# Kernel tuning notes

Hardware: AMD Instinct MI355X
Metric: run time of the kernel (lower is better)

The kernel has to match this reference:

```python
import jax, jax.numpy as jnp
import numpy as np

NHEAD, D_K, D_V, D_MODEL = 16, 64, 64, 1024
B, LQ, LK = 2, 2048, 2048
LN_EPS = 1e-6


def setup_inputs() -> dict:
    key = jax.random.key(0)
    ks = jax.random.split(key, 12)
    s = 0.02
    return {
        "q": jax.random.normal(ks[0], (B, LQ, D_MODEL), jnp.float32),
        "k": jax.random.normal(ks[1], (B, LK, D_MODEL), jnp.float32),
        "v": jax.random.normal(ks[2], (B, LK, D_MODEL), jnp.float32),
        "mask": jax.random.randint(ks[3], (B, LQ, LK), 0, 2, jnp.int32),
        "mean": jax.random.uniform(ks[4], (B, LK), jnp.float32, 0.5, 1.5),
        "std": jax.random.uniform(ks[5], (B, LK), jnp.float32, -0.5, 0.5),
        "w_qs": jax.random.normal(ks[6], (D_MODEL, NHEAD * D_K), jnp.float32) * s,
        "w_ks": jax.random.normal(ks[7], (D_MODEL, NHEAD * D_K), jnp.float32) * s,
        "w_vs": jax.random.normal(ks[8], (D_MODEL, NHEAD * D_V), jnp.float32) * s,
        "w_fc": jax.random.normal(ks[9], (NHEAD * D_V, D_MODEL), jnp.float32) * s,
        "ln_gamma": jnp.ones((D_MODEL,), jnp.float32),
        "ln_beta": jnp.zeros((D_MODEL,), jnp.float32),
    }


def _layer_norm(x, gamma, beta):
    mu = jnp.mean(x, axis=-1, keepdims=True)
    var = jnp.mean(jnp.square(x - mu), axis=-1, keepdims=True)
    return (x - mu) * jax.lax.rsqrt(var + LN_EPS) * gamma + beta


def reference(q, k, v, mask, mean, std, w_qs, w_ks, w_vs, w_fc, ln_gamma, ln_beta):
    residual = q
    # projections -> [B, H, L, d]
    qh = (q @ w_qs).reshape(B, LQ, NHEAD, D_K).transpose(0, 2, 1, 3)
    kh = (k @ w_ks).reshape(B, LK, NHEAD, D_K).transpose(0, 2, 1, 3)
    vh = (v @ w_vs).reshape(B, LK, NHEAD, D_V).transpose(0, 2, 1, 3)
    # scores with affine modification: (QK^T * mean + std) / sqrt(d_k)
    attn = jnp.einsum("bhqd,bhkd->bhqk", qh, kh)
    attn = (attn * mean[:, None, None, :] + std[:, None, None, :]) / jnp.sqrt(jnp.float32(D_K))
    attn = jnp.where(mask[:, None, :, :] == 0, jnp.float32(-1e9), attn)
    attn = jax.nn.softmax(attn, axis=-1)
    out = jnp.einsum("bhqk,bhkd->bhqd", attn, vh)  # [B,H,Lq,Dv]
    out = out.transpose(0, 2, 1, 3).reshape(B, LQ, NHEAD * D_V)
    out = out @ w_fc + residual
    return _layer_norm(out, ln_gamma, ln_beta)
```

## Files before the change

### kernel.cpp

```cpp
#include <hip/hip_runtime.h>
#include <math.h>

#define NHEAD 16
#define DK 64
#define DMODEL 1024
#define BB 2
#define LQ 2048
#define LK 2048
#define MROWS (BB * LQ)

typedef __attribute__((ext_vector_type(8))) short short8v;
typedef __attribute__((ext_vector_type(4))) float f32x4;
typedef __attribute__((ext_vector_type(16))) float f32x16;

__device__ __forceinline__ ushort f2bf(float x) {
  uint u = __builtin_bit_cast(uint, x);
  u += 0x7FFFu + ((u >> 16) & 1u);
  return (ushort)(u >> 16);
}
__device__ __forceinline__ float bf2f(ushort h) {
  return __builtin_bit_cast(float, ((uint)h) << 16);
}

template <int MODE>
__global__ __launch_bounds__(256, 2) void gemm_mfma(
    const float* __restrict__ A, const float* __restrict__ W,
    float* __restrict__ out, const float* __restrict__ res) {
  __shared__ __align__(16) ushort As_hi[128 * 32], As_lo[128 * 32];
  __shared__ __align__(16) ushort Bs_hi[128 * 32], Bs_lo[128 * 32];

  const int t = threadIdx.x;
  const int ln = t & 63, wv = t >> 6;
  const int wm = wv >> 1, wn = wv & 1;
  const int n0 = blockIdx.x * 128, m0 = blockIdx.y * 128;

  const int am = t & 127, akg = t >> 7;
  const int bn = t & 127, bkg = t >> 7;

  const float* Ap = A + (size_t)(m0 + am) * 1024 + akg * 16;
  const float* Wp = W + (size_t)(bkg * 16) * 1024 + n0 + bn;

  float4 apf[4];
  float wpf[16];
#pragma unroll
  for (int q = 0; q < 4; ++q) apf[q] = *(const float4*)&Ap[q * 4];
#pragma unroll
  for (int j = 0; j < 16; ++j) wpf[j] = Wp[(size_t)j * 1024];

  f32x4 acc[4][4];
#pragma unroll
  for (int i = 0; i < 4; ++i)
#pragma unroll
    for (int j = 0; j < 4; ++j)
#pragma unroll
      for (int r = 0; r < 4; ++r) acc[i][j][r] = 0.f;

  for (int k0 = 0; k0 < 1024; k0 += 32) {
    __syncthreads();
    {
      ushort h8[16], l8[16];
#pragma unroll
      for (int q = 0; q < 4; ++q)
#pragma unroll
        for (int c = 0; c < 4; ++c) {
          float x = apf[q][c];
          ushort hb = f2bf(x);
          h8[q * 4 + c] = hb;
          l8[q * 4 + c] = f2bf(x - bf2f(hb));
        }
      const int sw = (am >> 1) & 3;
      short8v va0, va1, vb0, vb1;
#pragma unroll
      for (int i = 0; i < 8; ++i) {
        va0[i] = (short)h8[i]; va1[i] = (short)h8[8 + i];
        vb0[i] = (short)l8[i]; vb1[i] = (short)l8[8 + i];
      }
      *(short8v*)&As_hi[am * 32 + ((akg * 2) ^ sw) * 8] = va0;
      *(short8v*)&As_hi[am * 32 + ((akg * 2 + 1) ^ sw) * 8] = va1;
      *(short8v*)&As_lo[am * 32 + ((akg * 2) ^ sw) * 8] = vb0;
      *(short8v*)&As_lo[am * 32 + ((akg * 2 + 1) ^ sw) * 8] = vb1;
    }
    {
      ushort h8[16], l8[16];
#pragma unroll
      for (int j = 0; j < 16; ++j) {
        float x = wpf[j];
        ushort hb = f2bf(x);
        h8[j] = hb;
        l8[j] = f2bf(x - bf2f(hb));
      }
      const int sw = (bn >> 1) & 3;
      short8v va0, va1, vb0, vb1;
#pragma unroll
      for (int i = 0; i < 8; ++i) {
        va0[i] = (short)h8[i]; va1[i] = (short)h8[8 + i];
        vb0[i] = (short)l8[i]; vb1[i] = (short)l8[8 + i];
      }
      *(short8v*)&Bs_hi[bn * 32 + ((bkg * 2) ^ sw) * 8] = va0;
      *(short8v*)&Bs_hi[bn * 32 + ((bkg * 2 + 1) ^ sw) * 8] = va1;
      *(short8v*)&Bs_lo[bn * 32 + ((bkg * 2) ^ sw) * 8] = vb0;
      *(short8v*)&Bs_lo[bn * 32 + ((bkg * 2 + 1) ^ sw) * 8] = vb1;
    }
    __syncthreads();

    if (k0 + 32 < 1024) {
#pragma unroll
      for (int q = 0; q < 4; ++q) apf[q] = *(const float4*)&Ap[k0 + 32 + q * 4];
#pragma unroll
      for (int j = 0; j < 16; ++j) wpf[j] = Wp[(size_t)(k0 + 32 + j) * 1024];
    }

    short8v ah[4], al[4], bh[4], bl[4];
#pragma unroll
    for (int mf = 0; mf < 4; ++mf) {
      const int mr = wm * 64 + mf * 16 + (ln & 15);
      const int sl = (ln >> 4) ^ ((mr >> 1) & 3);
      ah[mf] = *(const short8v*)&As_hi[mr * 32 + sl * 8];
      al[mf] = *(const short8v*)&As_lo[mr * 32 + sl * 8];
    }
#pragma unroll
    for (int nf = 0; nf < 4; ++nf) {
      const int nr = wn * 64 + nf * 16 + (ln & 15);
      const int sl = (ln >> 4) ^ ((nr >> 1) & 3);
      bh[nf] = *(const short8v*)&Bs_hi[nr * 32 + sl * 8];
      bl[nf] = *(const short8v*)&Bs_lo[nr * 32 + sl * 8];
    }
#pragma unroll
    for (int mi = 0; mi < 4; ++mi)
#pragma unroll
      for (int ni = 0; ni < 4; ++ni) {
        acc[mi][ni] = __builtin_amdgcn_mfma_f32_16x16x32_bf16(
            ah[mi], bh[ni], acc[mi][ni], 0, 0, 0);
        acc[mi][ni] = __builtin_amdgcn_mfma_f32_16x16x32_bf16(
            al[mi], bh[ni], acc[mi][ni], 0, 0, 0);
        acc[mi][ni] = __builtin_amdgcn_mfma_f32_16x16x32_bf16(
            ah[mi], bl[ni], acc[mi][ni], 0, 0, 0);
      }
  }

#pragma unroll
  for (int mi = 0; mi < 4; ++mi)
#pragma unroll
    for (int ni = 0; ni < 4; ++ni) {
      const int ng = n0 + wn * 64 + ni * 16 + (ln & 15);
#pragma unroll
      for (int r = 0; r < 4; ++r) {
        const int mg = m0 + wm * 64 + mi * 16 + (ln >> 4) * 4 + r;
        if (MODE == 0) {
          const int h = ng >> 6, d = ng & 63;
          const int bb = mg >> 11, l = mg & (LQ - 1);
          out[((size_t)(bb * NHEAD + h) * LQ + l) * 64 + d] = acc[mi][ni][r];
        } else {
          out[(size_t)mg * 1024 + ng] =
              acc[mi][ni][r] + res[(size_t)mg * 1024 + ng];
        }
      }
    }
}

__global__ __launch_bounds__(256, 2) void attn_mfma(
    const float* __restrict__ Qh, const float* __restrict__ Kh,
    const float* __restrict__ Vh, const int* __restrict__ mask,
    const float* __restrict__ mean, const float* __restrict__ stdv,
    float* __restrict__ ao) {
  __shared__ __align__(16) ushort Ks_hi[32 * 64], Ks_lo[32 * 64];
  __shared__ __align__(16) ushort VT_hi[64 * 40], VT_lo[64 * 40];
  __shared__ __align__(16) ushort P_hi[4][32 * 40], P_lo[4][32 * 40];
  __shared__ float sc_lds[4][32];

  const int t = threadIdx.x;
  const int w = t >> 6, ln = t & 63;
  const int lq = ln & 31;
  const int hi5 = ln >> 5;

  const int q0 = blockIdx.x * 128 + w * 32;
  const int h = blockIdx.y, b = blockIdx.z;

  const float* Qb = Qh + (size_t)(b * NHEAD + h) * LK * 64;
  const float* Kb = Kh + (size_t)(b * NHEAD + h) * LK * 64;
  const float* Vb = Vh + (size_t)(b * NHEAD + h) * LK * 64;

  short8v qf_h[4], qf_l[4];
#pragma unroll
  for (int ds = 0; ds < 4; ++ds) {
    float4 x0 = *(const float4*)&Qb[(size_t)(q0 + lq) * 64 + ds * 16 + hi5 * 8];
    float4 x1 =
        *(const float4*)&Qb[(size_t)(q0 + lq) * 64 + ds * 16 + hi5 * 8 + 4];
    float xv[8] = {x0.x, x0.y, x0.z, x0.w, x1.x, x1.y, x1.z, x1.w};
#pragma unroll
    for (int j = 0; j < 8; ++j) {
      ushort hb = f2bf(xv[j]);
      qf_h[ds][j] = (short)hb;
      qf_l[ds][j] = (short)f2bf(xv[j] - bf2f(hb));
    }
  }

  const int skr = t >> 3, sds = t & 7;
  const int svd = t & 63, svk = t >> 6;

  float4 kpf0 = *(const float4*)&Kb[(size_t)skr * 64 + sds * 8];
  float4 kpf1 = *(const float4*)&Kb[(size_t)skr * 64 + sds * 8 + 4];
  float vpf[8];
#pragma unroll
  for (int j = 0; j < 8; ++j) vpf[j] = Vb[(size_t)(svk * 8 + j) * 64 + svd];

  f32x16 Oa[2];
#pragma unroll
  for (int dt = 0; dt < 2; ++dt)
#pragma unroll
    for (int r = 0; r < 16; ++r) Oa[dt][r] = 0.f;
  float mrun = -INFINITY, lrun = 0.f;

  for (int k0 = 0; k0 < LK; k0 += 32) {
    __syncthreads();
    {
      ushort h8[8], l8[8];
      float kv[8] = {kpf0.x, kpf0.y, kpf0.z, kpf0.w,
                     kpf1.x, kpf1.y, kpf1.z, kpf1.w};
#pragma unroll
      for (int j = 0; j < 8; ++j) {
        ushort hb = f2bf(kv[j]);
        h8[j] = hb;
        l8[j] = f2bf(kv[j] - bf2f(hb));
      }
      short8v vh_, vl_;
#pragma unroll
      for (int i = 0; i < 8; ++i) { vh_[i] = (short)h8[i]; vl_[i] = (short)l8[i]; }
      const int ssl = sds ^ (skr & 7);
      *(short8v*)&Ks_hi[skr * 64 + ssl * 8] = vh_;
      *(short8v*)&Ks_lo[skr * 64 + ssl * 8] = vl_;
    }
    {
      short8v vh_, vl_;
#pragma unroll
      for (int j = 0; j < 8; ++j) {
        ushort hb = f2bf(vpf[j]);
        vh_[j] = (short)hb;
        vl_[j] = (short)f2bf(vpf[j] - bf2f(hb));
      }
      *(short8v*)&VT_hi[svd * 40 + svk * 8] = vh_;
      *(short8v*)&VT_lo[svd * 40 + svk * 8] = vl_;
    }
    __syncthreads();

    float4 mn[4], sd[4];
    int4 mk[4];
#pragma unroll
    for (int g = 0; g < 4; ++g) {
      const int kb = k0 + 8 * g + 4 * hi5;
      mn[g] = *(const float4*)&mean[(size_t)b * LK + kb];
      sd[g] = *(const float4*)&stdv[(size_t)b * LK + kb];
      mk[g] = *(const int4*)&mask[((size_t)b * LQ + q0 + lq) * LK + kb];
    }

    if (k0 + 32 < LK) {
      kpf0 = *(const float4*)&Kb[(size_t)(k0 + 32 + skr) * 64 + sds * 8];
      kpf1 = *(const float4*)&Kb[(size_t)(k0 + 32 + skr) * 64 + sds * 8 + 4];
#pragma unroll
      for (int j = 0; j < 8; ++j)
        vpf[j] = Vb[(size_t)(k0 + 32 + svk * 8 + j) * 64 + svd];
    }

    f32x16 S;
#pragma unroll
    for (int r = 0; r < 16; ++r) S[r] = 0.f;
#pragma unroll
    for (int ds = 0; ds < 4; ++ds) {
      const int dsl = (ds * 2 + hi5) ^ (lq & 7);
      short8v kf_h = *(const short8v*)&Ks_hi[lq * 64 + dsl * 8];
      short8v kf_l = *(const short8v*)&Ks_lo[lq * 64 + dsl * 8];
      S = __builtin_amdgcn_mfma_f32_32x32x16_bf16(kf_h, qf_h[ds], S, 0, 0, 0);
      S = __builtin_amdgcn_mfma_f32_32x32x16_bf16(kf_l, qf_h[ds], S, 0, 0, 0);
      S = __builtin_amdgcn_mfma_f32_32x32x16_bf16(kf_h, qf_l[ds], S, 0, 0, 0);
    }

    float p[16];
    float tmax = -INFINITY;
#pragma unroll
    for (int r = 0; r < 16; ++r) {
      const int g = r >> 2, j = r & 3;
      float v = fmaf(S[r], ((const float*)&mn[g])[j] * 0.125f,
                     ((const float*)&sd[g])[j] * 0.125f);
      v = (((const int*)&mk[g])[j] == 0) ? -1e9f : v;
      p[r] = v;
      tmax = fmaxf(tmax, v);
    }
    tmax = fmaxf(tmax, __shfl_xor(tmax, 32, 64));
    const float mnew = fmaxf(mrun, tmax);
    const float scl = __expf(mrun - mnew);
    float psum = 0.f;
#pragma unroll
    for (int r = 0; r < 16; ++r) {
      p[r] = __expf(p[r] - mnew);
      psum += p[r];
    }
    psum += __shfl_xor(psum, 32, 64);
    lrun = lrun * scl + psum;
    mrun = mnew;

#pragma unroll
    for (int r = 0; r < 16; r += 2) {
      const int k = (r & 3) + 8 * (r >> 2) + 4 * hi5;
      ushort h0 = f2bf(p[r]), h1 = f2bf(p[r + 1]);
      *(uint*)&P_hi[w][lq * 40 + k] = (uint)h0 | ((uint)h1 << 16);
      ushort l0 = f2bf(p[r] - bf2f(h0)), l1 = f2bf(p[r + 1] - bf2f(h1));
      *(uint*)&P_lo[w][lq * 40 + k] = (uint)l0 | ((uint)l1 << 16);
    }
    sc_lds[w][lq] = scl;

    float4 s4[4];
#pragma unroll
    for (int g = 0; g < 4; ++g)
      s4[g] = *(const float4*)&sc_lds[w][8 * g + 4 * hi5];
#pragma unroll
    for (int dt = 0; dt < 2; ++dt)
#pragma unroll
      for (int r = 0; r < 16; ++r) Oa[dt][r] *= ((const float*)&s4[r >> 2])[r & 3];

#pragma unroll
    for (int dt = 0; dt < 2; ++dt)
#pragma unroll
      for (int ki = 0; ki < 2; ++ki) {
        short8v pah = *(const short8v*)&P_hi[w][lq * 40 + ki * 16 + hi5 * 8];
        short8v pal = *(const short8v*)&P_lo[w][lq * 40 + ki * 16 + hi5 * 8];
        short8v vbh =
            *(const short8v*)&VT_hi[(dt * 32 + lq) * 40 + ki * 16 + hi5 * 8];
        short8v vbl =
            *(const short8v*)&VT_lo[(dt * 32 + lq) * 40 + ki * 16 + hi5 * 8];
        Oa[dt] = __builtin_amdgcn_mfma_f32_32x32x16_bf16(pah, vbh, Oa[dt], 0, 0, 0);
        Oa[dt] = __builtin_amdgcn_mfma_f32_32x32x16_bf16(pal, vbh, Oa[dt], 0, 0, 0);
        Oa[dt] = __builtin_amdgcn_mfma_f32_32x32x16_bf16(pah, vbl, Oa[dt], 0, 0, 0);
      }
  }

  sc_lds[w][lq] = 1.0f / lrun;
  float4 iv[4];
#pragma unroll
  for (int g = 0; g < 4; ++g)
    iv[g] = *(const float4*)&sc_lds[w][8 * g + 4 * hi5];
#pragma unroll
  for (int dt = 0; dt < 2; ++dt)
#pragma unroll
    for (int r = 0; r < 16; ++r) {
      const int ql = (r & 3) + 8 * (r >> 2) + 4 * hi5;
      const float v = Oa[dt][r] * ((const float*)&iv[r >> 2])[r & 3];
      ao[(size_t)(b * LQ + q0 + ql) * DMODEL + h * 64 + dt * 32 + lq] = v;
    }
}

__global__ __launch_bounds__(256) void ln_kernel(float* __restrict__ io,
                                                 const float* __restrict__ gamma,
                                                 const float* __restrict__ beta) {
  const int row = blockIdx.x;
  const int t = threadIdx.x;
  float* base = io + (size_t)row * DMODEL;
  float4 x = *(const float4*)&base[t << 2];
  float s = x.x + x.y + x.z + x.w;
#pragma unroll
  for (int xm = 1; xm < 64; xm <<= 1) s += __shfl_xor(s, xm, 64);
  __shared__ float part[4];
  __shared__ float smu, svar;
  if ((t & 63) == 0) part[t >> 6] = s;
  __syncthreads();
  if (t == 0) smu = (part[0] + part[1] + part[2] + part[3]) * (1.0f / DMODEL);
  __syncthreads();
  const float mu = smu;
  const float d0 = x.x - mu, d1 = x.y - mu, d2 = x.z - mu, d3 = x.w - mu;
  float s2 = d0 * d0 + d1 * d1 + d2 * d2 + d3 * d3;
#pragma unroll
  for (int xm = 1; xm < 64; xm <<= 1) s2 += __shfl_xor(s2, xm, 64);
  if ((t & 63) == 0) part[t >> 6] = s2;
  __syncthreads();
  if (t == 0) svar = (part[0] + part[1] + part[2] + part[3]) * (1.0f / DMODEL);
  __syncthreads();
  const float inv = rsqrtf(svar + 1e-6f);
  float4 g = *(const float4*)&gamma[t << 2];
  float4 be = *(const float4*)&beta[t << 2];
  float4 o;
  o.x = d0 * inv * g.x + be.x;
  o.y = d1 * inv * g.y + be.y;
  o.z = d2 * inv * g.z + be.z;
  o.w = d3 * inv * g.w + be.w;
  *(float4*)&base[t << 2] = o;
}

extern "C" void kernel_launch(void* const* d_in, const int* in_sizes, int n_in,
                              void* d_out, int out_size, void* d_ws,
                              size_t ws_size, hipStream_t stream) {
  const float* q = (const float*)d_in[0];
  const float* k = (const float*)d_in[1];
  const float* v = (const float*)d_in[2];
  const int* mask = (const int*)d_in[3];
  const float* mean = (const float*)d_in[4];
  const float* stdv = (const float*)d_in[5];
  const float* w_qs = (const float*)d_in[6];
  const float* w_ks = (const float*)d_in[7];
  const float* w_vs = (const float*)d_in[8];
  const float* w_fc = (const float*)d_in[9];
  const float* gamma = (const float*)d_in[10];
  const float* beta = (const float*)d_in[11];
  float* out = (float*)d_out;

  const size_t HSZ = (size_t)BB * NHEAD * LQ * DK;
  float* qh = (float*)d_ws;
  float* kh = qh + HSZ;
  float* vh = kh + HSZ;
  float* ao = vh + HSZ;

  dim3 blk(256);
  dim3 gg(DMODEL / 128, MROWS / 128);
  gemm_mfma<0><<<gg, blk, 0, stream>>>(q, w_qs, qh, nullptr);
  gemm_mfma<0><<<gg, blk, 0, stream>>>(k, w_ks, kh, nullptr);
  gemm_mfma<0><<<gg, blk, 0, stream>>>(v, w_vs, vh, nullptr);
  attn_mfma<<<dim3(LQ / 128, NHEAD, BB), blk, 0, stream>>>(qh, kh, vh, mask,
                                                           mean, stdv, ao);
  gemm_mfma<1><<<gg, blk, 0, stream>>>(ao, w_fc, out, q);
  ln_kernel<<<MROWS, blk, 0, stream>>>(out, gamma, beta);
}
```

Before: 564.3 us.

## Precompute bf16 hi/lo splits in global memory and pre-transpose weights and V

Adds conversion kernels that split the fp32 activations and weights into bf16 hi/lo planes once, with the weights also transposed so GEMM B tiles load as contiguous vectors. The projection GEMMs now write bf16 hi/lo outputs directly, V is written transposed for the attention kernel, and attention writes its output as hi/lo for the final GEMM. This removes the repeated per-tile fp32-to-bf16 splitting and the strided scalar loads inside the GEMM and attention inner loops. The cost is extra kernel launches, additional conversion passes over the inputs and weights on every call, and scattered 2-byte stores in the epilogues.

```diff
diff --git a/kernel.cpp b/kernel.cpp
--- a/kernel.cpp
+++ b/kernel.cpp
@@ -22,10 +22,66 @@
   return __builtin_bit_cast(float, ((uint)h) << 16);
 }
 
+__global__ __launch_bounds__(256) void conv_x(const float* __restrict__ x,
+                                              ushort* __restrict__ hi,
+                                              ushort* __restrict__ lo, int n4) {
+  for (int i = blockIdx.x * blockDim.x + threadIdx.x; i < n4;
+       i += gridDim.x * blockDim.x) {
+    float4 v = ((const float4*)x)[i];
+    ushort4 h, l;
+    h.x = f2bf(v.x); l.x = f2bf(v.x - bf2f(h.x));
+    h.y = f2bf(v.y); l.y = f2bf(v.y - bf2f(h.y));
+    h.z = f2bf(v.z); l.z = f2bf(v.z - bf2f(h.z));
+    h.w = f2bf(v.w); l.w = f2bf(v.w - bf2f(h.w));
+    ((ushort4*)hi)[i] = h;
+    ((ushort4*)lo)[i] = l;
+  }
+}
+
+__global__ __launch_bounds__(256) void conv_wT(
+    const float* __restrict__ w0, const float* __restrict__ w1,
+    const float* __restrict__ w2, const float* __restrict__ w3,
+    ushort* __restrict__ hiB, ushort* __restrict__ loB) {
+  const float* W = blockIdx.z == 0 ? w0
+                   : blockIdx.z == 1 ? w1
+                   : blockIdx.z == 2 ? w2 : w3;
+  ushort* hi = hiB + (size_t)blockIdx.z * DMODEL * DMODEL;
+  ushort* lo = loB + (size_t)blockIdx.z * DMODEL * DMODEL;
+  __shared__ ushort Th[64][66], Tl[64][66];
+  const int t = threadIdx.x;
+  const int n0 = blockIdx.x * 64, k0 = blockIdx.y * 64;
+  const int r = t >> 4, c4 = (t & 15) << 2;
+#pragma unroll
+  for (int p = 0; p < 4; ++p) {
+    const int kr = r + p * 16;
+    float4 v = *(const float4*)&W[(size_t)(k0 + kr) * DMODEL + n0 + c4];
+    ushort h;
+    h = f2bf(v.x); Th[c4 + 0][kr] = h; Tl[c4 + 0][kr] = f2bf(v.x - bf2f(h));
+    h = f2bf(v.y); Th[c4 + 1][kr] = h; Tl[c4 + 1][kr] = f2bf(v.y - bf2f(h));
+    h = f2bf(v.z); Th[c4 + 2][kr] = h; Tl[c4 + 2][kr] = f2bf(v.z - bf2f(h));
+    h = f2bf(v.w); Th[c4 + 3][kr] = h; Tl[c4 + 3][kr] = f2bf(v.w - bf2f(h));
+  }
+  __syncthreads();
+  const int n = t >> 2, g = t & 3;
+  uint uh[8], ul[8];
+#pragma unroll
+  for (int j = 0; j < 8; ++j) {
+    uh[j] = *(const uint*)&Th[n][g * 16 + 2 * j];
+    ul[j] = *(const uint*)&Tl[n][g * 16 + 2 * j];
+  }
+  const size_t ob = (size_t)(n0 + n) * DMODEL + k0 + g * 16;
+  *(uint4*)&hi[ob] = make_uint4(uh[0], uh[1], uh[2], uh[3]);
+  *(uint4*)&hi[ob + 8] = make_uint4(uh[4], uh[5], uh[6], uh[7]);
+  *(uint4*)&lo[ob] = make_uint4(ul[0], ul[1], ul[2], ul[3]);
+  *(uint4*)&lo[ob + 8] = make_uint4(ul[4], ul[5], ul[6], ul[7]);
+}
+
 template <int MODE>
 __global__ __launch_bounds__(256, 2) void gemm_mfma(
-    const float* __restrict__ A, const float* __restrict__ W,
-    float* __restrict__ out, const float* __restrict__ res) {
+    const ushort* __restrict__ Ah, const ushort* __restrict__ Al,
+    const ushort* __restrict__ Bh, const ushort* __restrict__ Bl,
+    ushort* __restrict__ Oh, ushort* __restrict__ Ol,
+    float* __restrict__ outF, const float* __restrict__ res) {
   __shared__ __align__(16) ushort As_hi[128 * 32], As_lo[128 * 32];
   __shared__ __align__(16) ushort Bs_hi[128 * 32], Bs_lo[128 * 32];
 
@@ -35,17 +91,17 @@
   const int n0 = blockIdx.x * 128, m0 = blockIdx.y * 128;
 
   const int am = t & 127, akg = t >> 7;
-  const int bn = t & 127, bkg = t >> 7;
-
-  const float* Ap = A + (size_t)(m0 + am) * 1024 + akg * 16;
-  const float* Wp = W + (size_t)(bkg * 16) * 1024 + n0 + bn;
-
-  float4 apf[4];
-  float wpf[16];
-#pragma unroll
-  for (int q = 0; q < 4; ++q) apf[q] = *(const float4*)&Ap[q * 4];
-#pragma unroll
-  for (int j = 0; j < 16; ++j) wpf[j] = Wp[(size_t)j * 1024];
+  const int bn = am, bkg = akg;
+
+  const ushort* Aph = Ah + (size_t)(m0 + am) * 1024 + akg * 16;
+  const ushort* Apl = Al + (size_t)(m0 + am) * 1024 + akg * 16;
+  const ushort* Bph = Bh + (size_t)(n0 + bn) * 1024 + bkg * 16;
+  const ushort* Bpl = Bl + (size_t)(n0 + bn) * 1024 + bkg * 16;
+
+  short8v ah0 = *(const short8v*)(Aph), ah1 = *(const short8v*)(Aph + 8);
+  short8v al0 = *(const short8v*)(Apl), al1 = *(const short8v*)(Apl + 8);
+  short8v bh0 = *(const short8v*)(Bph), bh1 = *(const short8v*)(Bph + 8);
+  short8v bl0 = *(const short8v*)(Bpl), bl1 = *(const short8v*)(Bpl + 8);
 
   f32x4 acc[4][4];
 #pragma unroll
@@ -54,87 +110,58 @@
     for (int j = 0; j < 4; ++j)
 #pragma unroll
       for (int r = 0; r < 4; ++r) acc[i][j][r] = 0.f;
+
+  const int swa = (am >> 1) & 3;
+  const int s0 = (akg * 2) ^ swa, s1 = (akg * 2 + 1) ^ swa;
 
   for (int k0 = 0; k0 < 1024; k0 += 32) {
     __syncthreads();
-    {
-      ushort h8[16], l8[16];
-#pragma unroll
-      for (int q = 0; q < 4; ++q)
-#pragma unroll
-        for (int c = 0; c < 4; ++c) {
-          float x = apf[q][c];
-          ushort hb = f2bf(x);
-          h8[q * 4 + c] = hb;
-          l8[q * 4 + c] = f2bf(x - bf2f(hb));
-        }
-      const int sw = (am >> 1) & 3;
-      short8v va0, va1, vb0, vb1;
-#pragma unroll
-      for (int i = 0; i < 8; ++i) {
-        va0[i] = (short)h8[i]; va1[i] = (short)h8[8 + i];
-        vb0[i] = (short)l8[i]; vb1[i] = (short)l8[8 + i];
-      }
-      *(short8v*)&As_hi[am * 32 + ((akg * 2) ^ sw) * 8] = va0;
-      *(short8v*)&As_hi[am * 32 + ((akg * 2 + 1) ^ sw) * 8] = va1;
-      *(short8v*)&As_lo[am * 32 + ((akg * 2) ^ sw) * 8] = vb0;
-      *(short8v*)&As_lo[am * 32 + ((akg * 2 + 1) ^ sw) * 8] = vb1;
-    }
-    {
-      ushort h8[16], l8[16];
-#pragma unroll
-      for (int j = 0; j < 16; ++j) {
-        float x = wpf[j];
-        ushort hb = f2bf(x);
-        h8[j] = hb;
-        l8[j] = f2bf(x - bf2f(hb));
-      }
-      const int sw = (bn >> 1) & 3;
-      short8v va0, va1, vb0, vb1;
-#pragma unroll
-      for (int i = 0; i < 8; ++i) {
-        va0[i] = (short)h8[i]; va1[i] = (short)h8[8 + i];
-        vb0[i] = (short)l8[i]; vb1[i] = (short)l8[8 + i];
-      }
-      *(short8v*)&Bs_hi[bn * 32 + ((bkg * 2) ^ sw) * 8] = va0;
-      *(short8v*)&Bs_hi[bn * 32 + ((bkg * 2 + 1) ^ sw) * 8] = va1;
-      *(short8v*)&Bs_lo[bn * 32 + ((bkg * 2) ^ sw) * 8] = vb0;
-      *(short8v*)&Bs_lo[bn * 32 + ((bkg * 2 + 1) ^ sw) * 8] = vb1;
-    }
+    *(short8v*)&As_hi[am * 32 + s0 * 8] = ah0;
+    *(short8v*)&As_hi[am * 32 + s1 * 8] = ah1;
+    *(short8v*)&As_lo[am * 32 + s0 * 8] = al0;
+    *(short8v*)&As_lo[am * 32 + s1 * 8] = al1;
+    *(short8v*)&Bs_hi[bn * 32 + s0 * 8] = bh0;
+    *(short8v*)&Bs_hi[bn * 32 + s1 * 8] = bh1;
+    *(short8v*)&Bs_lo[bn * 32 + s0 * 8] = bl0;
+    *(short8v*)&Bs_lo[bn * 32 + s1 * 8] = bl1;
     __syncthreads();
 
     if (k0 + 32 < 1024) {
-#pragma unroll
-      for (int q = 0; q < 4; ++q) apf[q] = *(const float4*)&Ap[k0 + 32 + q * 4];
-#pragma unroll
-      for (int j = 0; j < 16; ++j) wpf[j] = Wp[(size_t)(k0 + 32 + j) * 1024];
-    }
-
-    short8v ah[4], al[4], bh[4], bl[4];
+      ah0 = *(const short8v*)(Aph + k0 + 32);
+      ah1 = *(const short8v*)(Aph + k0 + 40);
+      al0 = *(const short8v*)(Apl + k0 + 32);
+      al1 = *(const short8v*)(Apl + k0 + 40);
+      bh0 = *(const short8v*)(Bph + k0 + 32);
+      bh1 = *(const short8v*)(Bph + k0 + 40);
+      bl0 = *(const short8v*)(Bpl + k0 + 32);
+      bl1 = *(const short8v*)(Bpl + k0 + 40);
+    }
+
+    short8v fah[4], fal[4], fbh[4], fbl[4];
 #pragma unroll
     for (int mf = 0; mf < 4; ++mf) {
       const int mr = wm * 64 + mf * 16 + (ln & 15);
       const int sl = (ln >> 4) ^ ((mr >> 1) & 3);
-      ah[mf] = *(const short8v*)&As_hi[mr * 32 + sl * 8];
-      al[mf] = *(const short8v*)&As_lo[mr * 32 + sl * 8];
+      fah[mf] = *(const short8v*)&As_hi[mr * 32 + sl * 8];
+      fal[mf] = *(const short8v*)&As_lo[mr * 32 + sl * 8];
     }
 #pragma unroll
     for (int nf = 0; nf < 4; ++nf) {
       const int nr = wn * 64 + nf * 16 + (ln & 15);
       const int sl = (ln >> 4) ^ ((nr >> 1) & 3);
-      bh[nf] = *(const short8v*)&Bs_hi[nr * 32 + sl * 8];
-      bl[nf] = *(const short8v*)&Bs_lo[nr * 32 + sl * 8];
+      fbh[nf] = *(const short8v*)&Bs_hi[nr * 32 + sl * 8];
+      fbl[nf] = *(const short8v*)&Bs_lo[nr * 32 + sl * 8];
     }
 #pragma unroll
     for (int mi = 0; mi < 4; ++mi)
 #pragma unroll
       for (int ni = 0; ni < 4; ++ni) {
         acc[mi][ni] = __builtin_amdgcn_mfma_f32_16x16x32_bf16(
-            ah[mi], bh[ni], acc[mi][ni], 0, 0, 0);
+            fah[mi], fbh[ni], acc[mi][ni], 0, 0, 0);
         acc[mi][ni] = __builtin_amdgcn_mfma_f32_16x16x32_bf16(
-            al[mi], bh[ni], acc[mi][ni], 0, 0, 0);
+            fal[mi], fbh[ni], acc[mi][ni], 0, 0, 0);
         acc[mi][ni] = __builtin_amdgcn_mfma_f32_16x16x32_bf16(
-            ah[mi], bl[ni], acc[mi][ni], 0, 0, 0);
+            fah[mi], fbl[ni], acc[mi][ni], 0, 0, 0);
       }
   }
 
@@ -146,23 +173,30 @@
 #pragma unroll
       for (int r = 0; r < 4; ++r) {
         const int mg = m0 + wm * 64 + mi * 16 + (ln >> 4) * 4 + r;
-        if (MODE == 0) {
+        const float val = acc[mi][ni][r];
+        if (MODE == 1) {
+          outF[(size_t)mg * 1024 + ng] = val + res[(size_t)mg * 1024 + ng];
+        } else {
           const int h = ng >> 6, d = ng & 63;
           const int bb = mg >> 11, l = mg & (LQ - 1);
-          out[((size_t)(bb * NHEAD + h) * LQ + l) * 64 + d] = acc[mi][ni][r];
-        } else {
-          out[(size_t)mg * 1024 + ng] =
-              acc[mi][ni][r] + res[(size_t)mg * 1024 + ng];
+          size_t idx;
+          if (MODE == 0) idx = ((size_t)(bb * NHEAD + h) * LQ + l) * 64 + d;
+          else           idx = ((size_t)(bb * NHEAD + h) * 64 + d) * LK + l;
+          const ushort hb = f2bf(val);
+          Oh[idx] = hb;
+          Ol[idx] = f2bf(val - bf2f(hb));
         }
       }
     }
 }
 
 __global__ __launch_bounds__(256, 2) void attn_mfma(
-    const float* __restrict__ Qh, const float* __restrict__ Kh,
-    const float* __restrict__ Vh, const int* __restrict__ mask,
-    const float* __restrict__ mean, const float* __restrict__ stdv,
-    float* __restrict__ ao) {
+    const ushort* __restrict__ Qhh, const ushort* __restrict__ Qhl,
+    const ushort* __restrict__ Khh, const ushort* __restrict__ Khl,
+    const ushort* __restrict__ VTh, const ushort* __restrict__ VTl,
+    const int* __restrict__ mask, const float* __restrict__ mean,
+    const float* __restrict__ stdv, ushort* __restrict__ AOh,
+    ushort* __restrict__ AOl) {
   __shared__ __align__(16) ushort Ks_hi[32 * 64], Ks_lo[32 * 64];
   __shared__ __align__(16) ushort VT_hi[64 * 40], VT_lo[64 * 40];
   __shared__ __align__(16) ushort P_hi[4][32 * 40], P_lo[4][32 * 40];
@@ -176,33 +210,30 @@
   const int q0 = blockIdx.x * 128 + w * 32;
   const int h = blockIdx.y, b = blockIdx.z;
 
-  const float* Qb = Qh + (size_t)(b * NHEAD + h) * LK * 64;
-  const float* Kb = Kh + (size_t)(b * NHEAD + h) * LK * 64;
-  const float* Vb = Vh + (size_t)(b * NHEAD + h) * LK * 64;
+  const size_t hb_ = (size_t)(b * NHEAD + h);
+  const ushort* Qh_ = Qhh + hb_ * LQ * 64;
+  const ushort* Ql_ = Qhl + hb_ * LQ * 64;
+  const ushort* Kh_ = Khh + hb_ * LK * 64;
+  const ushort* Kl_ = Khl + hb_ * LK * 64;
+  const ushort* Vh_ = VTh + hb_ * 64 * LK;
+  const ushort* Vl_ = VTl + hb_ * 64 * LK;
 
   short8v qf_h[4], qf_l[4];
 #pragma unroll
   for (int ds = 0; ds < 4; ++ds) {
-    float4 x0 = *(const float4*)&Qb[(size_t)(q0 + lq) * 64 + ds * 16 + hi5 * 8];
-    float4 x1 =
-        *(const float4*)&Qb[(size_t)(q0 + lq) * 64 + ds * 16 + hi5 * 8 + 4];
-    float xv[8] = {x0.x, x0.y, x0.z, x0.w, x1.x, x1.y, x1.z, x1.w};
-#pragma unroll
-    for (int j = 0; j < 8; ++j) {
-      ushort hb = f2bf(xv[j]);
-      qf_h[ds][j] = (short)hb;
-      qf_l[ds][j] = (short)f2bf(xv[j] - bf2f(hb));
-    }
+    const size_t off = (size_t)(q0 + lq) * 64 + ds * 16 + hi5 * 8;
+    qf_h[ds] = *(const short8v*)&Qh_[off];
+    qf_l[ds] = *(const short8v*)&Ql_[off];
   }
 
   const int skr = t >> 3, sds = t & 7;
-  const int svd = t & 63, svk = t >> 6;
-
-  float4 kpf0 = *(const float4*)&Kb[(size_t)skr * 64 + sds * 8];
-  float4 kpf1 = *(const float4*)&Kb[(size_t)skr * 64 + sds * 8 + 4];
-  float vpf[8];
-#pragma unroll
-  for (int j = 0; j < 8; ++j) vpf[j] = Vb[(size_t)(svk * 8 + j) * 64 + svd];
+  const int vd = t >> 2, vg = t & 3;
+  const int kslot = sds ^ (skr & 7);
+
+  short8v kp_h = *(const short8v*)&Kh_[(size_t)skr * 64 + sds * 8];
+  short8v kp_l = *(const short8v*)&Kl_[(size_t)skr * 64 + sds * 8];
+  short8v vp_h = *(const short8v*)&Vh_[(size_t)vd * LK + vg * 8];
+  short8v vp_l = *(const short8v*)&Vl_[(size_t)vd * LK + vg * 8];
 
   f32x16 Oa[2];
 #pragma unroll
@@ -213,34 +244,10 @@
 
   for (int k0 = 0; k0 < LK; k0 += 32) {
     __syncthreads();
-    {
-      ushort h8[8], l8[8];
-      float kv[8] = {kpf0.x, kpf0.y, kpf0.z, kpf0.w,
-                     kpf1.x, kpf1.y, kpf1.z, kpf1.w};
-#pragma unroll
-      for (int j = 0; j < 8; ++j) {
-        ushort hb = f2bf(kv[j]);
-        h8[j] = hb;
-        l8[j] = f2bf(kv[j] - bf2f(hb));
-      }
-      short8v vh_, vl_;
-#pragma unroll
-      for (int i = 0; i < 8; ++i) { vh_[i] = (short)h8[i]; vl_[i] = (short)l8[i]; }
-      const int ssl = sds ^ (skr & 7);
-      *(short8v*)&Ks_hi[skr * 64 + ssl * 8] = vh_;
-      *(short8v*)&Ks_lo[skr * 64 + ssl * 8] = vl_;
-    }
-    {
-      short8v vh_, vl_;
-#pragma unroll
-      for (int j = 0; j < 8; ++j) {
-        ushort hb = f2bf(vpf[j]);
-        vh_[j] = (short)hb;
-        vl_[j] = (short)f2bf(vpf[j] - bf2f(hb));
-      }
-      *(short8v*)&VT_hi[svd * 40 + svk * 8] = vh_;
-      *(short8v*)&VT_lo[svd * 40 + svk * 8] = vl_;
-    }
+    *(short8v*)&Ks_hi[skr * 64 + kslot * 8] = kp_h;
+    *(short8v*)&Ks_lo[skr * 64 + kslot * 8] = kp_l;
+    *(short8v*)&VT_hi[vd * 40 + vg * 8] = vp_h;
+    *(short8v*)&VT_lo[vd * 40 + vg * 8] = vp_l;
     __syncthreads();
 
     float4 mn[4], sd[4];
@@ -254,11 +261,10 @@
     }
 
     if (k0 + 32 < LK) {
-      kpf0 = *(const float4*)&Kb[(size_t)(k0 + 32 + skr) * 64 + sds * 8];
-      kpf1 = *(const float4*)&Kb[(size_t)(k0 + 32 + skr) * 64 + sds * 8 + 4];
-#pragma unroll
-      for (int j = 0; j < 8; ++j)
-        vpf[j] = Vb[(size_t)(k0 + 32 + svk * 8 + j) * 64 + svd];
+      kp_h = *(const short8v*)&Kh_[(size_t)(k0 + 32 + skr) * 64 + sds * 8];
+      kp_l = *(const short8v*)&Kl_[(size_t)(k0 + 32 + skr) * 64 + sds * 8];
+      vp_h = *(const short8v*)&Vh_[(size_t)vd * LK + k0 + 32 + vg * 8];
+      vp_l = *(const short8v*)&Vl_[(size_t)vd * LK + k0 + 32 + vg * 8];
     }
 
     f32x16 S;
@@ -344,7 +350,11 @@
     for (int r = 0; r < 16; ++r) {
       const int ql = (r & 3) + 8 * (r >> 2) + 4 * hi5;
       const float v = Oa[dt][r] * ((const float*)&iv[r >> 2])[r & 3];
-      ao[(size_t)(b * LQ + q0 + ql) * DMODEL + h * 64 + dt * 32 + lq] = v;
+      const size_t idx =
+          (size_t)(b * LQ + q0 + ql) * DMODEL + h * 64 + dt * 32 + lq;
+      const ushort hbv = f2bf(v);
+      AOh[idx] = hbv;
+      AOl[idx] = f2bf(v - bf2f(hbv));
     }
 }
 
@@ -401,19 +411,42 @@
   const float* beta = (const float*)d_in[11];
   float* out = (float*)d_out;
 
-  const size_t HSZ = (size_t)BB * NHEAD * LQ * DK;
-  float* qh = (float*)d_ws;
-  float* kh = qh + HSZ;
-  float* vh = kh + HSZ;
-  float* ao = vh + HSZ;
+  const size_t PL = (size_t)MROWS * DMODEL;
+  const size_t WL = (size_t)DMODEL * DMODEL;
+  ushort* wsp = (ushort*)d_ws;
+  ushort* qh_h = wsp;
+  ushort* qh_l = qh_h + PL;
+  ushort* kh_h = qh_l + PL;
+  ushort* kh_l = kh_h + PL;
+  ushort* vt_h = kh_l + PL;
+  ushort* vt_l = vt_h + PL;
+  ushort* wT_h = vt_l + PL;
+  ushort* wT_l = wT_h + 4 * WL;
+  ushort* xs_h = wT_l + 4 * WL;
+  ushort* xs_l = xs_h + PL;
+  ushort* ao_h = xs_h;
+  ushort* ao_l = xs_l;
 
   dim3 blk(256);
   dim3 gg(DMODEL / 128, MROWS / 128);
-  gemm_mfma<0><<<gg, blk, 0, stream>>>(q, w_qs, qh, nullptr);
-  gemm_mfma<0><<<gg, blk, 0, stream>>>(k, w_ks, kh, nullptr);
-  gemm_mfma<0><<<gg, blk, 0, stream>>>(v, w_vs, vh, nullptr);
-  attn_mfma<<<dim3(LQ / 128, NHEAD, BB), blk, 0, stream>>>(qh, kh, vh, mask,
-                                                           mean, stdv, ao);
-  gemm_mfma<1><<<gg, blk, 0, stream>>>(ao, w_fc, out, q);
+  const int n4 = MROWS * DMODEL / 4;
+
+  conv_wT<<<dim3(16, 16, 4), blk, 0, stream>>>(w_qs, w_ks, w_vs, w_fc, wT_h, wT_l);
+
+  conv_x<<<2048, blk, 0, stream>>>(q, xs_h, xs_l, n4);
+  gemm_mfma<0><<<gg, blk, 0, stream>>>(xs_h, xs_l, wT_h + 0 * WL, wT_l + 0 * WL,
+                                       qh_h, qh_l, nullptr, nullptr);
+  conv_x<<<2048, blk, 0, stream>>>(k, xs_h, xs_l, n4);
+  gemm_mfma<0><<<gg, blk, 0, stream>>>(xs_h, xs_l, wT_h + 1 * WL, wT_l + 1 * WL,
+                                       kh_h, kh_l, nullptr, nullptr);
+  conv_x<<<2048, blk, 0, stream>>>(v, xs_h, xs_l, n4);
+  gemm_mfma<2><<<gg, blk, 0, stream>>>(xs_h, xs_l, wT_h + 2 * WL, wT_l + 2 * WL,
+                                       vt_h, vt_l, nullptr, nullptr);
+
+  attn_mfma<<<dim3(LQ / 128, NHEAD, BB), blk, 0, stream>>>(
+      qh_h, qh_l, kh_h, kh_l, vt_h, vt_l, mask, mean, stdv, ao_h, ao_l);
+
+  gemm_mfma<1><<<gg, blk, 0, stream>>>(ao_h, ao_l, wT_h + 3 * WL, wT_l + 3 * WL,
+                                       nullptr, nullptr, out, q);
   ln_kernel<<<MROWS, blk, 0, stream>>>(out, gamma, beta);
 }
```

Result: faster. 547.4 us (-3.0%).
